# Optimization experiments

Measured on AMD Instinct MI355X. Metric: run time of the kernel, lower is better.

## Reference

```python
import jax, jax.numpy as jnp
import numpy as np


def setup_inputs() -> dict:
    key = jax.random.key(0)
    k1, k2, k3, k4, k5 = jax.random.split(key, 5)
    b, t_q, t_k = 4, 256, 1024
    qs, ms, n = 512, 512, 128
    return {
        "query": jax.random.normal(k1, (b, t_q, qs), dtype=jnp.float32),
        "keys": jax.random.normal(k2, (b, t_k, ms), dtype=jnp.float32),
        "Wq": jax.random.normal(k3, (qs, n), dtype=jnp.float32) * 0.05,
        "Wk": jax.random.normal(k4, (ms, n), dtype=jnp.float32) * 0.05,
        "linear_att": jax.random.normal(k5, (n,), dtype=jnp.float32) * 0.05,
    }


def reference(query, keys, Wq, Wk, linear_att):
    # projections: b t_q n and b t_k n
    att_query = jnp.einsum("bqd,dn->bqn", query, Wq)
    att_keys = jnp.einsum("bkd,dn->bkn", keys, Wk)
    # Bahdanau additive score: tanh(q + k) . v  -> b t_q t_k
    sum_qk = att_query[:, :, None, :] + att_keys[:, None, :, :]
    scores = jnp.einsum("bqkn,n->bqk", jnp.tanh(sum_qk), linear_att)
    weights = jax.nn.softmax(scores, axis=-1)
    context = jnp.einsum("bqk,bkd->bqd", weights, keys)
    return (context, weights)
```

## Files before the change

kernel.cpp:

```cpp
#include <hip/hip_runtime.h>

#define B 4
#define TQ 256
#define TK 1024
#define QS 512
#define NN 128

#define TANH_SCALE 2.8853900817779268f
#define LOG2E 1.4426950408889634f
#define CTX_ELEMS ((size_t)B * TQ * QS)

typedef unsigned short ushort_t;
typedef __attribute__((ext_vector_type(8))) short bfrag;
typedef __attribute__((ext_vector_type(4))) float ffrag;

union FragU { uint4 u; bfrag s; };

__device__ __forceinline__ float fast_exp2(float x) {
#if __has_builtin(__builtin_amdgcn_exp2f)
    return __builtin_amdgcn_exp2f(x);
#else
    return exp2f(x);
#endif
}
__device__ __forceinline__ float fast_rcp(float x) {
#if __has_builtin(__builtin_amdgcn_rcpf)
    return __builtin_amdgcn_rcpf(x);
#else
    return 1.0f / x;
#endif
}

__device__ __forceinline__ unsigned int pk_bf16(float a, float b) {
    unsigned int r;
    asm("v_cvt_pk_bf16_f32 %0, %1, %2" : "=v"(r) : "v"(a), "v"(b));
    return r;
}
__device__ __forceinline__ float lo16f(unsigned int u) { return __uint_as_float(u << 16); }
__device__ __forceinline__ float hi16f(unsigned int u) { return __uint_as_float(u & 0xffff0000u); }

__device__ __forceinline__ void split_frag(float4 a0, float4 a1, FragU& hi, FragU& lo) {
    const unsigned int h0 = pk_bf16(a0.x, a0.y), h1 = pk_bf16(a0.z, a0.w);
    const unsigned int h2 = pk_bf16(a1.x, a1.y), h3 = pk_bf16(a1.z, a1.w);
    const float l0 = a0.x - lo16f(h0), l1 = a0.y - hi16f(h0);
    const float l2 = a0.z - lo16f(h1), l3 = a0.w - hi16f(h1);
    const float l4 = a1.x - lo16f(h2), l5 = a1.y - hi16f(h2);
    const float l6 = a1.z - lo16f(h3), l7 = a1.w - hi16f(h3);
    hi.u = make_uint4(h0, h1, h2, h3);
    lo.u = make_uint4(pk_bf16(l0, l1), pk_bf16(l2, l3),
                      pk_bf16(l4, l5), pk_bf16(l6, l7));
}

__global__ __launch_bounds__(256) void transpose_split_kernel(
    const float* __restrict__ keys, const float* __restrict__ Wq,
    const float* __restrict__ Wk,
    ushort_t* __restrict__ keysT_hi, ushort_t* __restrict__ keysT_lo,
    ushort_t* __restrict__ WT_hi, ushort_t* __restrict__ WT_lo)
{
    __shared__ float t[32][33];
    const int tid = threadIdx.x;
    const int bid = blockIdx.x;
    const float* src; ushort_t *dh, *dl;
    int srcLD, dstLD, r0, c0;
    if (bid < 2048) {
        const int b = bid >> 9, tt = bid & 511;
        const int kt = tt & 31, dt = tt >> 5;
        src = keys + (size_t)b * TK * QS; srcLD = QS;
        dh = keysT_hi + (size_t)b * QS * TK;
        dl = keysT_lo + (size_t)b * QS * TK;
        dstLD = TK; r0 = kt * 32; c0 = dt * 32;
    } else {
        const int tt = bid - 2048;
        const int m = tt >> 6, t2 = tt & 63;
        const int kt = t2 & 15, nt = t2 >> 4;
        src = m ? Wk : Wq; srcLD = NN;
        dh = WT_hi + (size_t)m * NN * QS;
        dl = WT_lo + (size_t)m * NN * QS;
        dstLD = QS; r0 = kt * 32; c0 = nt * 32;
    }
    {
        const int rr = tid >> 3, cc = (tid & 7) * 4;
        const float4 v = *(const float4*)(src + (size_t)(r0 + rr) * srcLD + c0 + cc);
        t[rr][cc + 0] = v.x; t[rr][cc + 1] = v.y;
        t[rr][cc + 2] = v.z; t[rr][cc + 3] = v.w;
    }
    __syncthreads();
    {
        const int dr = tid >> 3, kc = (tid & 7) * 4;
        const float v0 = t[kc + 0][dr], v1 = t[kc + 1][dr];
        const float v2 = t[kc + 2][dr], v3 = t[kc + 3][dr];
        const unsigned int h01 = pk_bf16(v0, v1), h23 = pk_bf16(v2, v3);
        const float l0 = v0 - lo16f(h01), l1 = v1 - hi16f(h01);
        const float l2 = v2 - lo16f(h23), l3 = v3 - hi16f(h23);
        const unsigned int L01 = pk_bf16(l0, l1), L23 = pk_bf16(l2, l3);
        const size_t o = (size_t)(c0 + dr) * dstLD + r0 + kc;
        uint2 h; h.x = h01; h.y = h23;
        uint2 L; L.x = L01; L.y = L23;
        *(uint2*)(dh + o) = h;
        *(uint2*)(dl + o) = L;
    }
}

__global__ __launch_bounds__(256) void proj_mfma_kernel(
    const float* __restrict__ query, const float* __restrict__ keys,
    const ushort_t* __restrict__ WT_hi, const ushort_t* __restrict__ WT_lo,
    float* __restrict__ attq, float* __restrict__ attkT)
{
    __shared__ float As[4][16][36];
    const int tid = threadIdx.x, lane = tid & 63, w = tid >> 6;
    const int r0 = blockIdx.x * 32;
    const bool isq = (r0 < B * TQ);
    const float* Abase = isq ? (query + (size_t)r0 * QS)
                             : (keys + (size_t)(r0 - B * TQ) * QS);
    const ushort_t* BH = WT_hi + (isq ? 0 : (size_t)NN * QS);
    const ushort_t* BL = WT_lo + (isq ? 0 : (size_t)NN * QS);
    const int rb = w >> 1;
    const int nb0 = (w & 1) * 64;
    const int frow = lane & 15, fg = lane >> 4;
    const float* Arow = Abase + (size_t)(rb * 16) * QS;

    ffrag acc[4] = {};
    #pragma unroll 2
    for (int kb = 0; kb < QS; kb += 32) {
        FragU bh[4], bl[4];
        #pragma unroll
        for (int nb = 0; nb < 4; ++nb) {
            const size_t off = (size_t)(nb0 + nb * 16 + frow) * QS + kb + fg * 8;
            bh[nb].u = *(const uint4*)(BH + off);
            bl[nb].u = *(const uint4*)(BL + off);
        }
        #pragma unroll
        for (int it = 0; it < 2; ++it) {
            const int f = lane + it * 64;
            const int rr = f >> 3, cc = f & 7;
            *(float4*)&As[w][rr][cc * 4] =
                *(const float4*)(Arow + (size_t)rr * QS + kb + cc * 4);
        }
        const float4 a0 = *(const float4*)&As[w][frow][fg * 8];
        const float4 a1 = *(const float4*)&As[w][frow][fg * 8 + 4];
        FragU ah, al;
        split_frag(a0, a1, ah, al);
        #pragma unroll
        for (int nb = 0; nb < 4; ++nb) {
            acc[nb] = __builtin_amdgcn_mfma_f32_16x16x32_bf16(al.s, bh[nb].s, acc[nb], 0, 0, 0);
            acc[nb] = __builtin_amdgcn_mfma_f32_16x16x32_bf16(ah.s, bl[nb].s, acc[nb], 0, 0, 0);
            acc[nb] = __builtin_amdgcn_mfma_f32_16x16x32_bf16(ah.s, bh[nb].s, acc[nb], 0, 0, 0);
        }
    }

    const int orow = rb * 16 + fg * 4;
    if (isq) {
        #pragma unroll
        for (int nb = 0; nb < 4; ++nb) {
            const int n = nb0 + nb * 16 + frow;
            #pragma unroll
            for (int r = 0; r < 4; ++r)
                attq[(size_t)(r0 + orow + r) * NN + n] =
                    fast_exp2(acc[nb][r] * TANH_SCALE);
        }
    } else {
        const int rk = r0 - B * TQ;
        const int bb = rk >> 10;
        const int kk = (rk & 1023) + orow;
        #pragma unroll
        for (int nb = 0; nb < 4; ++nb) {
            const int n = nb0 + nb * 16 + frow;
            float4 o;
            o.x = fast_exp2(acc[nb][0] * TANH_SCALE);
            o.y = fast_exp2(acc[nb][1] * TANH_SCALE);
            o.z = fast_exp2(acc[nb][2] * TANH_SCALE);
            o.w = fast_exp2(acc[nb][3] * TANH_SCALE);
            *(float4*)(attkT + (size_t)bb * NN * TK + (size_t)n * TK + kk) = o;
        }
    }
}

__global__ __launch_bounds__(256) void score_softmax_kernel(
    const float* __restrict__ attq, const float* __restrict__ attkT,
    const float* __restrict__ vatt, float* __restrict__ wout)
{
    __shared__ float eqs[2][128];
    __shared__ float nv2[128];
    __shared__ float red[2][8];

    const int tid = threadIdx.x;
    const int b = blockIdx.x >> 7;
    const int q0 = (blockIdx.x & 127) * 2;

    if (tid < 128) {
        eqs[0][tid] = attq[((size_t)b * TQ + q0) * NN + tid];
        nv2[tid] = -2.0f * vatt[tid];
    } else {
        eqs[1][tid & 127] = attq[((size_t)b * TQ + q0 + 1) * NN + (tid & 127)];
    }
    __syncthreads();

    const float* kt = attkT + (size_t)b * NN * TK + (size_t)tid * 4;
    float s[2][4] = {};

    #pragma unroll 8
    for (int n = 0; n < 128; ++n) {
        const float4 a = *(const float4*)(kt + (size_t)n * TK);
        const float e0 = eqs[0][n], e1 = eqs[1][n], nv = nv2[n];
        const float av[4] = {a.x, a.y, a.z, a.w};
        #pragma unroll
        for (int rr = 0; rr < 4; ++rr) {
            const float r0 = fast_rcp(fmaf(av[rr], e0, 1.0f));
            s[0][rr] = fmaf(nv, r0, s[0][rr]);
            const float r1 = fast_rcp(fmaf(av[rr], e1, 1.0f));
            s[1][rr] = fmaf(nv, r1, s[1][rr]);
        }
    }

    const int lane = tid & 63, wid = tid >> 6;
    #pragma unroll
    for (int qq = 0; qq < 2; ++qq) {
        float mm = fmaxf(fmaxf(s[qq][0], s[qq][1]), fmaxf(s[qq][2], s[qq][3]));
        #pragma unroll
        for (int off = 32; off > 0; off >>= 1)
            mm = fmaxf(mm, __shfl_xor(mm, off, 64));
        if (lane == 0) red[qq][wid] = mm;
    }
    __syncthreads();
    float m[2];
    m[0] = fmaxf(fmaxf(red[0][0], red[0][1]), fmaxf(red[0][2], red[0][3]));
    m[1] = fmaxf(fmaxf(red[1][0], red[1][1]), fmaxf(red[1][2], red[1][3]));

    float e[2][4];
    #pragma unroll
    for (int qq = 0; qq < 2; ++qq) {
        float ls = 0.f;
        #pragma unroll
        for (int i = 0; i < 4; ++i) {
            e[qq][i] = fast_exp2((s[qq][i] - m[qq]) * LOG2E);
            ls += e[qq][i];
        }
        #pragma unroll
        for (int off = 32; off > 0; off >>= 1)
            ls += __shfl_xor(ls, off, 64);
        if (lane == 0) red[qq][4 + wid] = ls;
    }
    __syncthreads();
    #pragma unroll
    for (int qq = 0; qq < 2; ++qq) {
        const float S = red[qq][4] + red[qq][5] + red[qq][6] + red[qq][7];
        const float inv = fast_rcp(S);
        float4 w4;
        w4.x = e[qq][0] * inv; w4.y = e[qq][1] * inv;
        w4.z = e[qq][2] * inv; w4.w = e[qq][3] * inv;
        *(float4*)(wout + ((size_t)b * TQ + q0 + qq) * TK + (size_t)tid * 4) = w4;
    }
}

__global__ __launch_bounds__(256) void context_mfma_kernel(
    const float* __restrict__ wts, const ushort_t* __restrict__ KTh,
    const ushort_t* __restrict__ KTl, float* __restrict__ ctxp)
{
    __shared__ float As[4][16][36];
    const int tid = threadIdx.x, lane = tid & 63, w = tid >> 6;
    const int bid = blockIdx.x;
    const int ks = bid & 3, dt = (bid >> 2) & 3;
    const int qt = (bid >> 4) & 7, b = bid >> 7;
    const int rb = w >> 1, nb0 = (w & 1) * 64;
    const int frow = lane & 15, fg = lane >> 4;

    const float* Arow = wts + ((size_t)b * TQ + qt * 32 + rb * 16) * TK + ks * 256;
    const ushort_t* BH = KTh + ((size_t)b * QS + dt * 128) * TK + ks * 256;
    const ushort_t* BL = KTl + ((size_t)b * QS + dt * 128) * TK + ks * 256;

    ffrag acc[4] = {};
    #pragma unroll 2
    for (int kb = 0; kb < 256; kb += 32) {
        FragU bh[4], bl[4];
        #pragma unroll
        for (int nb = 0; nb < 4; ++nb) {
            const size_t off = (size_t)(nb0 + nb * 16 + frow) * TK + kb + fg * 8;
            bh[nb].u = *(const uint4*)(BH + off);
            bl[nb].u = *(const uint4*)(BL + off);
        }
        #pragma unroll
        for (int it = 0; it < 2; ++it) {
            const int f = lane + it * 64, rr = f >> 3, cc = f & 7;
            *(float4*)&As[w][rr][cc * 4] =
                *(const float4*)(Arow + (size_t)rr * TK + kb + cc * 4);
        }
        const float4 a0 = *(const float4*)&As[w][frow][fg * 8];
        const float4 a1 = *(const float4*)&As[w][frow][fg * 8 + 4];
        FragU ah, al;
        split_frag(a0, a1, ah, al);
        #pragma unroll
        for (int nb = 0; nb < 4; ++nb) {
            acc[nb] = __builtin_amdgcn_mfma_f32_16x16x32_bf16(al.s, bh[nb].s, acc[nb], 0, 0, 0);
            acc[nb] = __builtin_amdgcn_mfma_f32_16x16x32_bf16(ah.s, bl[nb].s, acc[nb], 0, 0, 0);
            acc[nb] = __builtin_amdgcn_mfma_f32_16x16x32_bf16(ah.s, bh[nb].s, acc[nb], 0, 0, 0);
        }
    }

    const int qrow = qt * 32 + rb * 16 + fg * 4;
    float* op = ctxp + (size_t)ks * CTX_ELEMS
              + ((size_t)b * TQ + qrow) * QS + dt * 128 + nb0 + frow;
    #pragma unroll
    for (int nb = 0; nb < 4; ++nb) {
        #pragma unroll
        for (int r = 0; r < 4; ++r)
            op[(size_t)r * QS + nb * 16] = acc[nb][r];
    }
}

__global__ __launch_bounds__(256) void reduce_kernel(
    const float4* __restrict__ ctxp, float4* __restrict__ ctx)
{
    const size_t idx = (size_t)blockIdx.x * 256 + threadIdx.x;
    const size_t stride = CTX_ELEMS / 4;
    const float4 a = ctxp[idx];
    const float4 b = ctxp[idx + stride];
    const float4 c = ctxp[idx + 2 * stride];
    const float4 d = ctxp[idx + 3 * stride];
    float4 o;
    o.x = (a.x + b.x) + (c.x + d.x);
    o.y = (a.y + b.y) + (c.y + d.y);
    o.z = (a.z + b.z) + (c.z + d.z);
    o.w = (a.w + b.w) + (c.w + d.w);
    ctx[idx] = o;
}

extern "C" void kernel_launch(void* const* d_in, const int* in_sizes, int n_in,
                              void* d_out, int out_size, void* d_ws, size_t ws_size,
                              hipStream_t stream) {
    const float* query = (const float*)d_in[0];
    const float* keys  = (const float*)d_in[1];
    const float* Wq    = (const float*)d_in[2];
    const float* Wk    = (const float*)d_in[3];
    const float* vatt  = (const float*)d_in[4];

    float* ctx = (float*)d_out;
    float* wts = ctx + CTX_ELEMS;

    float* attq  = (float*)d_ws;
    float* attkT = attq + (size_t)B * TQ * NN;
    float* ctxp  = attkT + (size_t)B * NN * TK;
    ushort_t* keysT_hi = (ushort_t*)(ctxp + 4 * CTX_ELEMS);
    ushort_t* keysT_lo = keysT_hi + (size_t)B * QS * TK;
    ushort_t* WT_hi    = keysT_lo + (size_t)B * QS * TK;
    ushort_t* WT_lo    = WT_hi + (size_t)2 * NN * QS;

    hipLaunchKernelGGL(transpose_split_kernel, dim3(2176), dim3(256), 0, stream,
                       keys, Wq, Wk, keysT_hi, keysT_lo, WT_hi, WT_lo);
    hipLaunchKernelGGL(proj_mfma_kernel, dim3(160), dim3(256), 0, stream,
                       query, keys, WT_hi, WT_lo, attq, attkT);
    hipLaunchKernelGGL(score_softmax_kernel, dim3(B * TQ / 2), dim3(256), 0,
                       stream, attq, attkT, vatt, wts);
    hipLaunchKernelGGL(context_mfma_kernel, dim3(512), dim3(256), 0, stream,
                       wts, keysT_hi, keysT_lo, ctxp);
    hipLaunchKernelGGL(reduce_kernel, dim3((unsigned)(CTX_ELEMS / 4 / 256)), dim3(256), 0,
                       stream, (const float4*)ctxp, (float4*)ctx);
}
```

Before: 137.7 us.

## Fuse keys transpose-split into projection and drop split-K context reduction

Moves the bf16 hi/lo transpose-split of keys into the projection kernel, reusing the keys tile already staged in shared memory, so the separate keys transpose pass and its extra read of keys disappear. The context GEMM no longer splits K four ways. Each block now covers the full key length over a narrower 64-column output tile and writes final results directly, which removes the partial-sum buffer and the reduce kernel. In exchange, the context kernel has only 256 blocks with long serial K loops and reads weights straight from global memory without LDS staging, and half of the key-projection waves do extra fold work.

```diff
diff --git a/kernel.cpp b/kernel.cpp
--- a/kernel.cpp
+++ b/kernel.cpp
@@ -51,36 +51,22 @@
                       pk_bf16(l4, l5), pk_bf16(l6, l7));
 }
 
-__global__ __launch_bounds__(256) void transpose_split_kernel(
-    const float* __restrict__ keys, const float* __restrict__ Wq,
-    const float* __restrict__ Wk,
-    ushort_t* __restrict__ keysT_hi, ushort_t* __restrict__ keysT_lo,
+__global__ __launch_bounds__(256) void transpose_w_kernel(
+    const float* __restrict__ Wq, const float* __restrict__ Wk,
     ushort_t* __restrict__ WT_hi, ushort_t* __restrict__ WT_lo)
 {
     __shared__ float t[32][33];
     const int tid = threadIdx.x;
     const int bid = blockIdx.x;
-    const float* src; ushort_t *dh, *dl;
-    int srcLD, dstLD, r0, c0;
-    if (bid < 2048) {
-        const int b = bid >> 9, tt = bid & 511;
-        const int kt = tt & 31, dt = tt >> 5;
-        src = keys + (size_t)b * TK * QS; srcLD = QS;
-        dh = keysT_hi + (size_t)b * QS * TK;
-        dl = keysT_lo + (size_t)b * QS * TK;
-        dstLD = TK; r0 = kt * 32; c0 = dt * 32;
-    } else {
-        const int tt = bid - 2048;
-        const int m = tt >> 6, t2 = tt & 63;
-        const int kt = t2 & 15, nt = t2 >> 4;
-        src = m ? Wk : Wq; srcLD = NN;
-        dh = WT_hi + (size_t)m * NN * QS;
-        dl = WT_lo + (size_t)m * NN * QS;
-        dstLD = QS; r0 = kt * 32; c0 = nt * 32;
-    }
+    const int m = bid >> 6, t2 = bid & 63;
+    const int kt = t2 & 15, nt = t2 >> 4;
+    const float* src = m ? Wk : Wq;
+    ushort_t* dh = WT_hi + (size_t)m * NN * QS;
+    ushort_t* dl = WT_lo + (size_t)m * NN * QS;
+    const int r0 = kt * 32, c0 = nt * 32;
     {
         const int rr = tid >> 3, cc = (tid & 7) * 4;
-        const float4 v = *(const float4*)(src + (size_t)(r0 + rr) * srcLD + c0 + cc);
+        const float4 v = *(const float4*)(src + (size_t)(r0 + rr) * NN + c0 + cc);
         t[rr][cc + 0] = v.x; t[rr][cc + 1] = v.y;
         t[rr][cc + 2] = v.z; t[rr][cc + 3] = v.w;
     }
@@ -93,7 +79,7 @@
         const float l0 = v0 - lo16f(h01), l1 = v1 - hi16f(h01);
         const float l2 = v2 - lo16f(h23), l3 = v3 - hi16f(h23);
         const unsigned int L01 = pk_bf16(l0, l1), L23 = pk_bf16(l2, l3);
-        const size_t o = (size_t)(c0 + dr) * dstLD + r0 + kc;
+        const size_t o = (size_t)(c0 + dr) * QS + r0 + kc;
         uint2 h; h.x = h01; h.y = h23;
         uint2 L; L.x = L01; L.y = L23;
         *(uint2*)(dh + o) = h;
@@ -104,7 +90,8 @@
 __global__ __launch_bounds__(256) void proj_mfma_kernel(
     const float* __restrict__ query, const float* __restrict__ keys,
     const ushort_t* __restrict__ WT_hi, const ushort_t* __restrict__ WT_lo,
-    float* __restrict__ attq, float* __restrict__ attkT)
+    float* __restrict__ attq, float* __restrict__ attkT,
+    ushort_t* __restrict__ keysT_hi, ushort_t* __restrict__ keysT_lo)
 {
     __shared__ float As[4][16][36];
     const int tid = threadIdx.x, lane = tid & 63, w = tid >> 6;
@@ -119,6 +106,14 @@
     const int frow = lane & 15, fg = lane >> 4;
     const float* Arow = Abase + (size_t)(rb * 16) * QS;
 
+    const int rk = isq ? 0 : (r0 - B * TQ);
+    const int bb = rk >> 10;
+    const int kf0 = (rk & 1023) + rb * 16;
+    const bool dofold = (!isq) && ((w & 1) == 0);
+    const int fd = lane & 31, fpl = lane >> 5;
+    ushort_t* fdst_base =
+        (fpl ? keysT_lo : keysT_hi) + (size_t)bb * QS * TK + kf0;
+
     ffrag acc[4] = {};
     #pragma unroll 2
     for (int kb = 0; kb < QS; kb += 32) {
@@ -140,6 +135,27 @@
         const float4 a1 = *(const float4*)&As[w][frow][fg * 8 + 4];
         FragU ah, al;
         split_frag(a0, a1, ah, al);
+
+        if (dofold) {
+            float v[16];
+            #pragma unroll
+            for (int j = 0; j < 16; ++j) v[j] = As[w][j][fd];
+            unsigned int o[8];
+            #pragma unroll
+            for (int j = 0; j < 8; ++j) {
+                const unsigned int h = pk_bf16(v[2 * j], v[2 * j + 1]);
+                const float l0 = v[2 * j]     - lo16f(h);
+                const float l1 = v[2 * j + 1] - hi16f(h);
+                const unsigned int L = pk_bf16(l0, l1);
+                o[j] = fpl ? L : h;
+            }
+            ushort_t* dst = fdst_base + (size_t)(kb + fd) * TK;
+            uint4 s0; s0.x = o[0]; s0.y = o[1]; s0.z = o[2]; s0.w = o[3];
+            uint4 s1; s1.x = o[4]; s1.y = o[5]; s1.z = o[6]; s1.w = o[7];
+            *(uint4*)(dst) = s0;
+            *(uint4*)(dst + 8) = s1;
+        }
+
         #pragma unroll
         for (int nb = 0; nb < 4; ++nb) {
             acc[nb] = __builtin_amdgcn_mfma_f32_16x16x32_bf16(al.s, bh[nb].s, acc[nb], 0, 0, 0);
@@ -159,8 +175,6 @@
                     fast_exp2(acc[nb][r] * TANH_SCALE);
         }
     } else {
-        const int rk = r0 - B * TQ;
-        const int bb = rk >> 10;
         const int kk = (rk & 1023) + orow;
         #pragma unroll
         for (int nb = 0; nb < 4; ++nb) {
@@ -254,74 +268,49 @@
 
 __global__ __launch_bounds__(256) void context_mfma_kernel(
     const float* __restrict__ wts, const ushort_t* __restrict__ KTh,
-    const ushort_t* __restrict__ KTl, float* __restrict__ ctxp)
+    const ushort_t* __restrict__ KTl, float* __restrict__ ctx)
 {
-    __shared__ float As[4][16][36];
     const int tid = threadIdx.x, lane = tid & 63, w = tid >> 6;
     const int bid = blockIdx.x;
-    const int ks = bid & 3, dt = (bid >> 2) & 3;
-    const int qt = (bid >> 4) & 7, b = bid >> 7;
-    const int rb = w >> 1, nb0 = (w & 1) * 64;
+    const int dt = bid & 7;
+    const int qt = (bid >> 3) & 7;
+    const int b  = bid >> 6;
+    const int rb = w >> 1, nb0 = (w & 1) * 32;
     const int frow = lane & 15, fg = lane >> 4;
 
-    const float* Arow = wts + ((size_t)b * TQ + qt * 32 + rb * 16) * TK + ks * 256;
-    const ushort_t* BH = KTh + ((size_t)b * QS + dt * 128) * TK + ks * 256;
-    const ushort_t* BL = KTl + ((size_t)b * QS + dt * 128) * TK + ks * 256;
-
-    ffrag acc[4] = {};
+    const float* Arow =
+        wts + ((size_t)b * TQ + qt * 32 + rb * 16 + frow) * TK + fg * 8;
+    const size_t boff = ((size_t)b * QS + dt * 64 + nb0 + frow) * TK + fg * 8;
+    const ushort_t* BH = KTh + boff;
+    const ushort_t* BL = KTl + boff;
+
+    ffrag acc[2] = {};
     #pragma unroll 2
-    for (int kb = 0; kb < 256; kb += 32) {
-        FragU bh[4], bl[4];
-        #pragma unroll
-        for (int nb = 0; nb < 4; ++nb) {
-            const size_t off = (size_t)(nb0 + nb * 16 + frow) * TK + kb + fg * 8;
-            bh[nb].u = *(const uint4*)(BH + off);
-            bl[nb].u = *(const uint4*)(BL + off);
-        }
-        #pragma unroll
-        for (int it = 0; it < 2; ++it) {
-            const int f = lane + it * 64, rr = f >> 3, cc = f & 7;
-            *(float4*)&As[w][rr][cc * 4] =
-                *(const float4*)(Arow + (size_t)rr * TK + kb + cc * 4);
-        }
-        const float4 a0 = *(const float4*)&As[w][frow][fg * 8];
-        const float4 a1 = *(const float4*)&As[w][frow][fg * 8 + 4];
+    for (int kb = 0; kb < TK; kb += 32) {
+        const float4 a0 = *(const float4*)(Arow + kb);
+        const float4 a1 = *(const float4*)(Arow + kb + 4);
         FragU ah, al;
         split_frag(a0, a1, ah, al);
         #pragma unroll
-        for (int nb = 0; nb < 4; ++nb) {
-            acc[nb] = __builtin_amdgcn_mfma_f32_16x16x32_bf16(al.s, bh[nb].s, acc[nb], 0, 0, 0);
-            acc[nb] = __builtin_amdgcn_mfma_f32_16x16x32_bf16(ah.s, bl[nb].s, acc[nb], 0, 0, 0);
-            acc[nb] = __builtin_amdgcn_mfma_f32_16x16x32_bf16(ah.s, bh[nb].s, acc[nb], 0, 0, 0);
+        for (int nb = 0; nb < 2; ++nb) {
+            FragU bh, bl;
+            bh.u = *(const uint4*)(BH + (size_t)nb * 16 * TK + kb);
+            bl.u = *(const uint4*)(BL + (size_t)nb * 16 * TK + kb);
+            acc[nb] = __builtin_amdgcn_mfma_f32_16x16x32_bf16(al.s, bh.s, acc[nb], 0, 0, 0);
+            acc[nb] = __builtin_amdgcn_mfma_f32_16x16x32_bf16(ah.s, bl.s, acc[nb], 0, 0, 0);
+            acc[nb] = __builtin_amdgcn_mfma_f32_16x16x32_bf16(ah.s, bh.s, acc[nb], 0, 0, 0);
         }
     }
 
     const int qrow = qt * 32 + rb * 16 + fg * 4;
-    float* op = ctxp + (size_t)ks * CTX_ELEMS
-              + ((size_t)b * TQ + qrow) * QS + dt * 128 + nb0 + frow;
+    const int dcol = dt * 64 + nb0 + frow;
+    float* op = ctx + ((size_t)b * TQ + qrow) * QS + dcol;
     #pragma unroll
-    for (int nb = 0; nb < 4; ++nb) {
+    for (int nb = 0; nb < 2; ++nb) {
         #pragma unroll
         for (int r = 0; r < 4; ++r)
             op[(size_t)r * QS + nb * 16] = acc[nb][r];
     }
-}
-
-__global__ __launch_bounds__(256) void reduce_kernel(
-    const float4* __restrict__ ctxp, float4* __restrict__ ctx)
-{
-    const size_t idx = (size_t)blockIdx.x * 256 + threadIdx.x;
-    const size_t stride = CTX_ELEMS / 4;
-    const float4 a = ctxp[idx];
-    const float4 b = ctxp[idx + stride];
-    const float4 c = ctxp[idx + 2 * stride];
-    const float4 d = ctxp[idx + 3 * stride];
-    float4 o;
-    o.x = (a.x + b.x) + (c.x + d.x);
-    o.y = (a.y + b.y) + (c.y + d.y);
-    o.z = (a.z + b.z) + (c.z + d.z);
-    o.w = (a.w + b.w) + (c.w + d.w);
-    ctx[idx] = o;
 }
 
 extern "C" void kernel_launch(void* const* d_in, const int* in_sizes, int n_in,
@@ -338,20 +327,18 @@
 
     float* attq  = (float*)d_ws;
     float* attkT = attq + (size_t)B * TQ * NN;
-    float* ctxp  = attkT + (size_t)B * NN * TK;
-    ushort_t* keysT_hi = (ushort_t*)(ctxp + 4 * CTX_ELEMS);
+    ushort_t* keysT_hi = (ushort_t*)(attkT + (size_t)B * NN * TK);
     ushort_t* keysT_lo = keysT_hi + (size_t)B * QS * TK;
     ushort_t* WT_hi    = keysT_lo + (size_t)B * QS * TK;
     ushort_t* WT_lo    = WT_hi + (size_t)2 * NN * QS;
 
-    hipLaunchKernelGGL(transpose_split_kernel, dim3(2176), dim3(256), 0, stream,
-                       keys, Wq, Wk, keysT_hi, keysT_lo, WT_hi, WT_lo);
+    hipLaunchKernelGGL(transpose_w_kernel, dim3(128), dim3(256), 0, stream,
+                       Wq, Wk, WT_hi, WT_lo);
     hipLaunchKernelGGL(proj_mfma_kernel, dim3(160), dim3(256), 0, stream,
-                       query, keys, WT_hi, WT_lo, attq, attkT);
+                       query, keys, WT_hi, WT_lo, attq, attkT,
+                       keysT_hi, keysT_lo);
     hipLaunchKernelGGL(score_softmax_kernel, dim3(B * TQ / 2), dim3(256), 0,
                        stream, attq, attkT, vatt, wts);
-    hipLaunchKernelGGL(context_mfma_kernel, dim3(512), dim3(256), 0, stream,
-                       wts, keysT_hi, keysT_lo, ctxp);
-    hipLaunchKernelGGL(reduce_kernel, dim3((unsigned)(CTX_ELEMS / 4 / 256)), dim3(256), 0,
-                       stream, (const float4*)ctxp, (float4*)ctx);
-}
+    hipLaunchKernelGGL(context_mfma_kernel, dim3(256), dim3(256), 0, stream,
+                       wts, keysT_hi, keysT_lo, ctx);
+}
```

Measured after the change: 138.6 us. No clear change (+0.6%).
